# Performance work log

Hardware: AMD Instinct MI355X
Metric: run time of the kernel (lower is better)

## Reference

```python
import jax, jax.numpy as jnp
import numpy as np
import math

N = 5000; K = 30; E = N * K
C_S, C_Z, C_A = 256, 128, 16
H, DH, P, L = 4, 64, 8, 4
NUM_AA = 21
NUM_RBF = 16; D_MIN, D_MAX = 2.0, 22.0
EPS = 1e-8

def _ln(x):
    mu = jnp.mean(x, -1, keepdims=True)
    var = jnp.mean((x - mu) ** 2, -1, keepdims=True)
    return (x - mu) * jax.lax.rsqrt(var + 1e-5)

def _inv_apply(rot, trans, x):
    # rigid invert_apply: R^T (x - t); rot [n,3,3], trans [n,3], x [n,p,3]
    return jnp.einsum('nji,npj->npi', rot, x - trans[:, None, :])

def _rbf(d):
    mu = jnp.linspace(D_MIN, D_MAX, NUM_RBF)
    sigma = (D_MAX - D_MIN) / NUM_RBF
    return jnp.exp(-(((d[..., None] - mu) / sigma) ** 2))

def _dihedral_feats(bb):
    X = bb.reshape(-1, 3)  # [3N,3] N,CA,C chain
    dX = X[1:] - X[:-1]
    U = dX / (jnp.linalg.norm(dX, axis=-1, keepdims=True) + EPS)
    u2, u1, u0 = U[:-2], U[1:-1], U[2:]
    n2 = jnp.cross(u2, u1); n2 = n2 / (jnp.linalg.norm(n2, axis=-1, keepdims=True) + EPS)
    n1 = jnp.cross(u1, u0); n1 = n1 / (jnp.linalg.norm(n1, axis=-1, keepdims=True) + EPS)
    cosD = jnp.clip(jnp.sum(n2 * n1, -1), -1 + 1e-7, 1 - 1e-7)
    D = jnp.sign(jnp.sum(u2 * n1, -1)) * jnp.arccos(cosD)
    D = jnp.pad(D, (1, 2)).reshape(-1, 3)  # [N,3]
    return jnp.concatenate([jnp.cos(D), jnp.sin(D)], -1)  # [N,6]

def _virtual_cb(n, ca, c):
    b = ca - n; cc = c - ca; a = jnp.cross(b, cc)
    return -0.58273431 * a + 0.56802827 * b - 0.54067466 * cc + ca

def _prep(seq, atom14, rot, trans, res_mask, mgm_mask, noising_mask, atom14_exists, edge_index, atom_tab):
    res_f = res_mask.astype(jnp.float32)
    mgm_f = mgm_mask.astype(jnp.float32)
    bb = atom14[:, :3]
    dih = _dihedral_feats(bb)
    seq_oh = jax.nn.one_hot(seq, NUM_AA)
    node_vec = _inv_apply(rot, trans, atom14[:, :4])  # [N,4,3]
    node_raw = jnp.concatenate([dih, mgm_f[:, None], seq_oh * mgm_f[:, None], node_vec.reshape(N, -1)], -1) * res_f[:, None]
    sc = jnp.where(jnp.arange(14) >= 4, mgm_f[:, None], 1.0)  # zero hidden side-chain atoms
    am_f = jnp.where(jnp.arange(14) >= 4, mgm_mask[:, None], atom14_exists).astype(jnp.float32)
    atom_raw = atom_tab[seq] * sc[..., None]  # [N,14,9]
    dsti, srci = edge_index[0], edge_index[1]
    nsrc = noising_mask[srci].astype(jnp.float32); ndst = noising_mask[dsti].astype(jnp.float32)
    cb = _virtual_cb(bb[:, 0], bb[:, 1], bb[:, 2])
    bb4 = jnp.concatenate([bb, cb[:, None]], 1)  # [N,4,3]
    dist = jnp.linalg.norm(bb4[srci][:, :, None] - bb4[dsti][:, None, :] + EPS, axis=-1)  # [E,4,4]
    rbf = _rbf(dist).reshape(E, -1)  # [E,256]
    dpos = (dsti - srci).astype(jnp.float32)
    freq = jnp.exp(jnp.arange(0, 16, 2, dtype=jnp.float32) * (-math.log(10000.0) / 16))
    ang = dpos[:, None] * freq
    pe = jnp.concatenate([jnp.cos(ang), jnp.sin(ang)], -1)  # [E,16]
    bb_local = _inv_apply(rot, trans, bb4)
    src_local = bb_local[srci].reshape(E, -1) * (1 - nsrc)[:, None]
    dst_in_src = jnp.einsum('eji,epj->epi', rot[srci], bb4[dsti] - trans[srci][:, None, :]).reshape(E, -1) * (1 - ndst)[:, None]
    edge_mask = res_mask[srci] & res_mask[dsti]
    edge_raw = jnp.concatenate([ndst[:, None], nsrc[:, None], seq_oh[srci] * (1 - nsrc)[:, None], seq_oh[dsti] * (1 - ndst)[:, None], rbf, pe, src_local, dst_in_src], -1) * edge_mask.astype(jnp.float32)[:, None]
    return node_raw, edge_raw, atom_raw, res_f, am_f, edge_mask

def _mlp3(x, W1, W2, W3):
    return _ln(jax.nn.relu(jax.nn.relu(x @ W1) @ W2) @ W3)

def _net(node_raw, edge_raw, atom_raw, res_f, am_f, edge_mask, rot, trans, edge_index, Wn1, Wn2, Wn3, Wez1, Wez2, Wez3, Wa1, Wa2, Wa3, Wq, Wk, Wv, Wqp, Wkp, Wb, gamma, Wo, Wau, Wt1, Wt2, Wne, We1, We2, Wp1, Wp2, Wmu, Wlv):
    s = _mlp3(node_raw, Wn1, Wn2, Wn3)    # [N,256]
    z = _mlp3(edge_raw, Wez1, Wez2, Wez3) # [E,128]
    af = _mlp3(atom_raw, Wa1, Wa2, Wa3)   # [N,14,16]
    dsti, srci = edge_index[0], edge_index[1]
    em_f = edge_mask.astype(jnp.float32)
    w_pt = math.sqrt(2.0 / (9 * P)); w_l = math.sqrt(1.0 / 3.0)
    for l in range(L):
        q = (s @ Wq[l]).reshape(N, H, DH); k = (s @ Wk[l]).reshape(N, H, DH); v = (s @ Wv[l]).reshape(N, H, DH)
        qp = (s @ Wqp[l]).reshape(N, H, P, 3); kp = (s @ Wkp[l]).reshape(N, H, P, 3)
        qg = jnp.einsum('nij,nhpj->nhpi', rot, qp) + trans[:, None, None, :]
        kg = jnp.einsum('nij,nhpj->nhpi', rot, kp) + trans[:, None, None, :]
        logits = (jnp.sum(q[dsti] * k[srci], -1) * (w_l / math.sqrt(DH))
                  + w_l * (z @ Wb[l])
                  - 0.5 * w_pt * jax.nn.softplus(gamma[l]) * jnp.sum((qg[dsti] - kg[srci]) ** 2, (-2, -1)))
        logits = jnp.where(edge_mask[:, None], logits, -1e9)
        m = jax.ops.segment_max(logits, dsti, num_segments=N)
        a = jnp.exp(logits - m[dsti]) * em_f[:, None]
        a = a / (jax.ops.segment_sum(a, dsti, num_segments=N) + 1e-9)[dsti]
        ov = jax.ops.segment_sum(a[..., None] * v[srci], dsti, num_segments=N).reshape(N, -1)
        og = jax.ops.segment_sum(a[..., None, None] * kg[srci], dsti, num_segments=N)
        ol = jnp.einsum('nji,nhpj->nhpi', rot, og - trans[:, None, None, :])
        on = jnp.sqrt(jnp.sum(ol ** 2, -1) + EPS)
        s = _ln(s + jnp.concatenate([ov, ol.reshape(N, -1), on.reshape(N, -1)], -1) @ Wo[l])
        af = _ln(af + jnp.concatenate([af, jnp.broadcast_to(s[:, None, :], (N, 14, C_S))], -1) @ Wau[l])
        s = _ln(s + jax.nn.relu(s @ Wt1[l]) @ Wt2[l]) * res_f[:, None]
        h = s @ Wne[l]
        z = _ln(jax.nn.relu(jnp.concatenate([z, h[dsti], h[srci]], -1) @ We1[l]) @ We2[l]) * em_f[:, None]
        af = _ln(af + jax.nn.relu(af @ Wp1[l]) @ Wp2[l]) * am_f[..., None]
    return jnp.concatenate([s @ Wmu, s @ Wlv], -1)  # [N,512] = [mu | logvar]

def setup_inputs():
    ks = jax.random.split(jax.random.key(0), 40)
    w = lambda i, shp: jax.random.normal(ks[i], shp, dtype=jnp.float32) * 0.02
    return {
        'seq': jax.random.randint(ks[0], (N,), 0, NUM_AA, dtype=jnp.int32),
        'atom14': jax.random.normal(ks[1], (N, 14, 3), dtype=jnp.float32) * 3.0,
        'rot': jax.random.normal(ks[2], (N, 3, 3), dtype=jnp.float32),
        'trans': jax.random.normal(ks[3], (N, 3), dtype=jnp.float32) * 3.0,
        'res_mask': jnp.ones((N,), dtype=bool),
        'mgm_mask': jax.random.bernoulli(ks[4], 0.5, (N,)),
        'noising_mask': jax.random.bernoulli(ks[5], 0.5, (N,)),
        'atom14_exists': jnp.ones((N, 14), dtype=bool),
        'edge_index': jax.random.randint(ks[6], (2, E), 0, N, dtype=jnp.int32),
        'atom_tab': jax.random.uniform(ks[7], (NUM_AA + 1, 14, 9), dtype=jnp.float32),
        'Wn1': w(8, (40, 512)), 'Wn2': w(9, (512, 512)), 'Wn3': w(10, (512, 256)),
        'Wez1': w(11, (340, 256)), 'Wez2': w(12, (256, 256)), 'Wez3': w(13, (256, 128)),
        'Wa1': w(14, (9, 32)), 'Wa2': w(15, (32, 32)), 'Wa3': w(16, (32, 16)),
        'Wq': w(17, (L, 256, 256)), 'Wk': w(18, (L, 256, 256)), 'Wv': w(19, (L, 256, 256)),
        'Wqp': w(20, (L, 256, H * P * 3)), 'Wkp': w(21, (L, 256, H * P * 3)),
        'Wb': w(22, (L, 128, H)), 'gamma': w(23, (L, H)),
        'Wo': w(24, (L, H * (DH + 4 * P), 256)), 'Wau': w(25, (L, C_A + C_S, C_A)),
        'Wt1': w(26, (L, 256, 256)), 'Wt2': w(27, (L, 256, 256)),
        'Wne': w(28, (L, 256, 128)), 'We1': w(29, (L, 384, 256)), 'We2': w(30, (L, 256, 128)),
        'Wp1': w(31, (L, 16, 16)), 'Wp2': w(32, (L, 16, 16)),
        'Wmu': w(33, (256, 256)), 'Wlv': w(34, (256, 256)),
    }

def reference(seq, atom14, rot, trans, res_mask, mgm_mask, noising_mask, atom14_exists, edge_index, atom_tab, Wn1, Wn2, Wn3, Wez1, Wez2, Wez3, Wa1, Wa2, Wa3, Wq, Wk, Wv, Wqp, Wkp, Wb, gamma, Wo, Wau, Wt1, Wt2, Wne, We1, We2, Wp1, Wp2, Wmu, Wlv):
    prep = _prep(seq, atom14, rot, trans, res_mask, mgm_mask, noising_mask, atom14_exists, edge_index, atom_tab)
    return _net(*prep, rot, trans, edge_index, Wn1, Wn2, Wn3, Wez1, Wez2, Wez3, Wa1, Wa2, Wa3, Wq, Wk, Wv, Wqp, Wkp, Wb, gamma, Wo, Wau, Wt1, Wt2, Wne, We1, We2, Wp1, Wp2, Wmu, Wlv)
```

## Files before the change

### kernel.cpp

```cpp
#include <hip/hip_runtime.h>
#include <hip/hip_bf16.h>

#define NR 5000
#define EE 150000
#define NA14 (NR*14)
#define EPSF 1e-8f

typedef unsigned short ushort;
typedef __attribute__((ext_vector_type(8))) short bf16x8;
typedef __attribute__((ext_vector_type(4))) float f32x4;

#define GLDS16(gp, lp) __builtin_amdgcn_global_load_lds( \
    (__attribute__((address_space(1))) void*)(gp), \
    (__attribute__((address_space(3))) void*)(lp), 16, 0, 0)

static __device__ __forceinline__ float wsum64(float v) {
#pragma unroll
  for (int o = 1; o < 64; o <<= 1) v += __shfl_xor(v, o, 64);
  return v;
}
static __device__ __forceinline__ ushort f2b(float f) {
  union { float f; unsigned u; } x; x.f = f;
  unsigned r = (x.u + 0x7FFF + ((x.u >> 16) & 1)) >> 16;
  return (ushort)r;
// ... 312 lines not shown
  const int ks0 = (sl - rl0 - (rl0 >> 2)) & 3;
  const int ks1 = (sl - rl1 - (rl1 >> 2)) & 3;
  int ar0 = bm + rl0; if (ar0 >= M) ar0 = M - 1;
  int ar1 = bm + rl1; if (ar1 >= M) ar1 = M - 1;
  const ushort* gA0 = A + (size_t)ar0 * lda + ks0 * 8;
  const ushort* gA1 = A + (size_t)ar1 * lda + ks1 * 8;
  const ushort* gB0 = BT + (size_t)(bn + rl0) * Kd + ks0 * 8;
  const ushort* gB1 = BT + (size_t)(bn + rl1) * Kd + ks1 * 8;

  auto stage = [&](int buf, int k0) {
    GLDS16(gA0 + k0, &As[buf][rl0][sl][0]);
    GLDS16(gB0 + k0, &Bs[buf][rl0][sl][0]);
    GLDS16(gA1 + k0, &As[buf][rl1][sl][0]);
    GLDS16(gB1 + k0, &Bs[buf][rl1][sl][0]);
  };

  f32x4 zero4 = {0.f, 0.f, 0.f, 0.f};
  f32x4 acc[4][4];
#pragma unroll
  for (int i = 0; i < 4; ++i)
#pragma unroll
    for (int j = 0; j < 4; ++j) acc[i][j] = zero4;

  stage(0, 0);
  asm volatile("s_waitcnt vmcnt(0)" ::: "memory");
  __builtin_amdgcn_s_barrier();

  const int nt = Kd >> 5;
  for (int t = 0; t < nt; ++t) {
    int cur = t & 1;
    if (t + 1 < nt) stage(cur ^ 1, (t + 1) << 5);
    {
      const int ksr = lane >> 4, lr = lane & 15;
      bf16x8 af[4], bf[4];
#pragma unroll
      for (int i = 0; i < 4; ++i) {
        int row = wm + i*16 + lr;
        int sa = (ksr + row + (row >> 2)) & 3;
        af[i] = *reinterpret_cast<const bf16x8*>(&As[cur][row][sa][0]);
      }
#pragma unroll
      for (int j = 0; j < 4; ++j) {
        int col = wn + j*16 + lr;
        int sb = (ksr + col + (col >> 2)) & 3;
        bf[j] = *reinterpret_cast<const bf16x8*>(&Bs[cur][col][sb][0]);
      }
#pragma unroll
      for (int i = 0; i < 4; ++i)
#pragma unroll
        for (int j = 0; j < 4; ++j)
          acc[i][j] = __builtin_amdgcn_mfma_f32_16x16x32_bf16(af[i], bf[j], acc[i][j], 0, 0, 0);
    }
    asm volatile("s_waitcnt vmcnt(0) lgkmcnt(0)" ::: "memory");
    __builtin_amdgcn_s_barrier();
  }

  int lr = lane & 15, lg = lane >> 4;
  if (LNZ) {
    float* stats = (float*)As;
#pragma unroll
    for (int i = 0; i < 4; ++i) {
#pragma unroll
      for (int rg = 0; rg < 4; ++rg) {
        float ps = 0.f, pq = 0.f;
#pragma unroll
        for (int j = 0; j < 4; ++j) {
          float v = b2f(f2b(acc[i][j][rg]));
          ps += v; pq += v * v;
        }
#pragma unroll
        for (int o = 1; o < 16; o <<= 1) {
          ps += __shfl_xor(ps, o, 64);
          pq += __shfl_xor(pq, o, 64);
        }
        if (lr == 0) {
          int row = wm + i*16 + lg*4 + rg;
          stats[(row * 2 + (wn >> 6)) * 2 + 0] = ps;
          stats[(row * 2 + (wn >> 6)) * 2 + 1] = pq;
        }
      }
    }
    __syncthreads();
#pragma unroll
    for (int i = 0; i < 4; ++i) {
#pragma unroll
      for (int rg = 0; rg < 4; ++rg) {
        int row = wm + i*16 + lg*4 + rg;
        int m = bm + row;
        float s0 = stats[(row*2 + 0)*2 + 0] + stats[(row*2 + 1)*2 + 0];
        float q0 = stats[(row*2 + 0)*2 + 1] + stats[(row*2 + 1)*2 + 1];
        float mu = s0 * (1.f / 128.f);
        float var = q0 * (1.f / 128.f) - mu * mu;
        float rs = rsqrtf(var + 1e-5f);
        if (m < M) {
          float sc = lnsc ? lnsc[m] : 1.f;
#pragma unroll
          for (int j = 0; j < 4; ++j) {
            int cc = wn + j*16 + lr;
            float v = b2f(f2b(acc[i][j][rg]));
            Cb[(size_t)m * 128 + cc] = f2b((v - mu) * rs * sc);
          }
        }
      }
    }
  } else if (PERMOUT) {
    const int pc = bn + wn + lr * 4;
#pragma unroll
    for (int i = 0; i < 4; ++i) {
#pragma unroll
      for (int rg = 0; rg < 4; ++rg) {
        int m = bm + wm + i*16 + lg*4 + rg;
        if (m >= M) continue;
        float v0 = acc[i][0][rg], v1 = acc[i][1][rg];
        float v2 = acc[i][2][rg], v3 = acc[i][3][rg];
        if (EPADD) {
          int de = dsti[m], se = srci[m];
          uint2 hd = *reinterpret_cast<const uint2*>(HD + (size_t)de * Ncols + pc);
          uint2 hs = *reinterpret_cast<const uint2*>(HS + (size_t)se * Ncols + pc);
          v0 += blo(hd.x) + blo(hs.x);
          v1 += bhi(hd.x) + bhi(hs.x);
          v2 += blo(hd.y) + blo(hs.y);
          v3 += bhi(hd.y) + bhi(hs.y);
        }
        if (RELU) {
          v0 = fmaxf(v0, 0.f); v1 = fmaxf(v1, 0.f);
          v2 = fmaxf(v2, 0.f); v3 = fmaxf(v3, 0.f);
        }
        uint2 p;
        p.x = (unsigned)f2b(v0) | ((unsigned)f2b(v1) << 16);
        p.y = (unsigned)f2b(v2) | ((unsigned)f2b(v3) << 16);
        *reinterpret_cast<uint2*>(Cb + (size_t)m * Ncols + pc) = p;
      }
    }
  } else {
#pragma unroll
    for (int i = 0; i < 4; ++i) {
#pragma unroll
      for (int rg = 0; rg < 4; ++rg) {
        int m = bm + wm + i*16 + lg*4 + rg;
        if (m >= M) continue;
#pragma unroll
        for (int j = 0; j < 4; ++j) {
          int cc = bn + wn + j*16 + lr;
          float v = acc[i][j][rg];
          if (RELU) v = fmaxf(v, 0.f);
          if (OUTBF) Cb[(size_t)m * Ncols + cc] = f2b(v);
          else       Cf[(size_t)m * Ncols + cc] = v;
        }
      }
    }
  }
}

__global__ void k_gemm(const float* __restrict__ A, const float* __restrict__ B,
                       float* __restrict__ C, int M, int Ncols, int Kd,
                       int ldc, int coff, int relu) {
  __shared__ float As[16][68];
  __shared__ float Bs[16][64];
  const int tid = threadIdx.x;
  const int bm = blockIdx.x * 64;
  const int bn = blockIdx.y * 64;
  const int tm = tid >> 4;
  const int tn = tid & 15;
  const int arow = tid >> 2;
  const int akq = (tid & 3) << 2;
  const int brow = tid >> 4;
  const int bcol = (tid & 15) << 2;
  float acc[4][4] = {{0.f}};
  const int am = bm + arow;
  for (int k0 = 0; k0 < Kd; k0 += 16) {
    float av[4];
#pragma unroll
    for (int j = 0; j < 4; ++j) {
      int k = k0 + akq + j;
      av[j] = (am < M && k < Kd) ? A[(size_t)am * Kd + k] : 0.f;
    }
#pragma unroll
    for (int j = 0; j < 4; ++j) As[akq + j][arow] = av[j];
    int kb = k0 + brow;
    float bv[4];
    if (kb < Kd) {
#pragma unroll
      for (int j = 0; j < 4; ++j) {
        int c = bn + bcol + j;
        bv[j] = (c < Ncols) ? B[(size_t)kb * Ncols + c] : 0.f;
      }
    } else { bv[0]=bv[1]=bv[2]=bv[3]=0.f; }
    *reinterpret_cast<float4*>(&Bs[brow][bcol]) = make_float4(bv[0],bv[1],bv[2],bv[3]);
    __syncthreads();
#pragma unroll
    for (int kk = 0; kk < 16; ++kk) {
      float4 a4 = *reinterpret_cast<const float4*>(&As[kk][tm << 2]);
      float4 b4 = *reinterpret_cast<const float4*>(&Bs[kk][tn << 2]);
      float aa[4] = {a4.x, a4.y, a4.z, a4.w};
      float bb[4] = {b4.x, b4.y, b4.z, b4.w};
#pragma unroll
      for (int i = 0; i < 4; ++i)
#pragma unroll
        for (int j = 0; j < 4; ++j)
          acc[i][j] = fmaf(aa[i], bb[j], acc[i][j]);
    }
    __syncthreads();
  }
#pragma unroll
  for (int i = 0; i < 4; ++i) {
    int m = bm + (tm << 2) + i;
    if (m >= M) continue;
#pragma unroll
    for (int j = 0; j < 4; ++j) {
      int c = bn + (tn << 2) + j;
      if (c >= Ncols) continue;
      float v = acc[i][j];
      if (relu) v = fmaxf(v, 0.f);
      C[(size_t)m * ldc + coff + c] = v;
    }
  }
}

__global__ void k_small_gemm(const float* __restrict__ A, const float* __restrict__ B,
                             float* __restrict__ C, int M, int Ncols, int Kd, int relu) {
  __shared__ float Ws[1024];
  int t = threadIdx.x;
  int nw = Kd * Ncols;
  for (int i = t; i < nw; i += 256) Ws[i] = B[i];
  __syncthreads();
  int rpb = 256 / Ncols;
  int r = blockIdx.x * rpb + t / Ncols;
  int c = t - (t / Ncols) * Ncols;
  if (r >= M || t >= rpb * Ncols) return;
  const float* a = A + (size_t)r * Kd;
  float s = 0.f;
  for (int k = 0; k < Kd; ++k) s = fmaf(a[k], Ws[k * Ncols + c], s);
  if (relu) s = fmaxf(s, 0.f);
  C[(size_t)r * Ncols + c] = s;
}

__global__ void k_ln(float* __restrict__ dst, ushort* __restrict__ dstb,
                     const float* __restrict__ res, const float* __restrict__ x,
                     const float* __restrict__ rowscale, int M) {
  int r = blockIdx.x * 4 + (threadIdx.x >> 6);
  if (r >= M) return;
  int l = threadIdx.x & 63;
  size_t base = (size_t)r * 256 + l * 4;
  float4 v = *reinterpret_cast<const float4*>(x + base);
  if (res) {
    float4 rv = *reinterpret_cast<const float4*>(res + base);
    v.x += rv.x; v.y += rv.y; v.z += rv.z; v.w += rv.w;
  }
  float s = wsum64(v.x + v.y + v.z + v.w);
  float mu = s * (1.f / 256.f);
  float d0 = v.x-mu, d1 = v.y-mu, d2 = v.z-mu, d3 = v.w-mu;
  float s2 = wsum64(d0*d0 + d1*d1 + d2*d2 + d3*d3);
  float rs = rsqrtf(s2 * (1.f / 256.f) + 1e-5f);
  float sc = rowscale ? rowscale[r] : 1.f;
  float o0 = d0*rs*sc, o1 = d1*rs*sc, o2 = d2*rs*sc, o3 = d3*rs*sc;
  *reinterpret_cast<float4*>(dst + base) = make_float4(o0, o1, o2, o3);
  if (dstb) {
    uint2 p;
    p.x = (unsigned)f2b(o0) | ((unsigned)f2b(o1) << 16);
    p.y = (unsigned)f2b(o2) | ((unsigned)f2b(o3) << 16);
    *reinterpret_cast<uint2*>(dstb + base) = p;
  }
}

__global__ void k_ln16(float* __restrict__ af, int M) {
  int r = blockIdx.x * 256 + threadIdx.x;
  if (r >= M) return;
  float x[16]; float s = 0.f;
#pragma unroll
  for (int j = 0; j < 16; ++j) { x[j] = af[(size_t)r*16 + j]; s += x[j]; }
  float mu = s * (1.f/16.f);
  float v = 0.f;
#pragma unroll
  for (int j = 0; j < 16; ++j) { float d = x[j]-mu; v += d*d; }
  float rs = rsqrtf(v * (1.f/16.f) + 1e-5f);
#pragma unroll
  for (int j = 0; j < 16; ++j) af[(size_t)r*16 + j] = (x[j]-mu)*rs;
}


__global__ void k_qg(const float* __restrict__ rot, const float* __restrict__ trans,
                     const float* __restrict__ pp,
                     float* __restrict__ qg, float* __restrict__ kg) {
  int idx = blockIdx.x * 256 + threadIdx.x;
  if (idx >= NR * 64) return;
  int n = idx >> 6; int w = (idx >> 5) & 1; int hp = idx & 31;
  const float* src = pp + (size_t)n*256 + (w ? 96 : 0) + hp*3;
  float* dstp = (w ? kg : qg) + (size_t)n*96 + hp*3;
  const float* R = rot + (size_t)n*9;
  const float* t = trans + (size_t)n*3;
  float s0 = src[0], s1 = src[1], s2 = src[2];
#pragma unroll
  for (int i = 0; i < 3; ++i)
    dstp[i] = R[i*3+0]*s0 + R[i*3+1]*s1 + R[i*3+2]*s2 + t[i];
}

__global__ __launch_bounds__(256) void k_attn2(
    const int* __restrict__ offs, const int* __restrict__ eord,
    const int* __restrict__ srci, const float* __restrict__ emf,
    const ushort* __restrict__ qkv, const ushort* __restrict__ z,
    const float* __restrict__ qg, const float* __restrict__ kg,
    const float* __restrict__ WbT, const float* __restrict__ coef,
    ushort* __restrict__ catb, float* __restrict__ og) {
  __shared__ float MS[2][2][8];
  __shared__ float AV[2][2][4][64];
  __shared__ float AG0[2][2][64];
  __shared__ float AG1[2][2][32];
  const int w = threadIdx.x >> 6;
  const int ns = w >> 1, half = w & 1;
  const int n = blockIdx.x * 2 + ns;
  const int l = threadIdx.x & 63;
  const int hh = l >> 4, t = l & 15;
  const int e0 = offs[n], e1 = offs[n+1];
  const float wl = 0.57735026918962576f;
  const float qk_scale = wl * 0.125f;
  uint2 qw = *reinterpret_cast<const uint2*>(qkv + n*768 + hh*64 + t*4);
  float q0 = blo(qw.x), q1 = bhi(qw.x), q2 = blo(qw.y), q3 = bhi(qw.y);
  float qg1 = qg[n*96 + hh*24 + t];
  float qg2 = (t < 8) ? qg[n*96 + hh*24 + t + 16] : 0.f;
  float cf = coef[hh];
  int hg0 = l / 24;
  int hg1 = (64 + l) / 24;

  float m[4] = {-1e30f,-1e30f,-1e30f,-1e30f};
  float den[4] = {0.f,0.f,0.f,0.f};
  float accv[4] = {0.f,0.f,0.f,0.f};
  float acg0 = 0.f, acg1 = 0.f;

  int i = e0 + half;
  int e = 0, s = 0;
  if (i < e1) {
    e = __builtin_amdgcn_readfirstlane(eord[i]);
    s = __builtin_amdgcn_readfirstlane(srci[e]);
  }
  for (; i < e1; i += 2) {
    int e_nxt = 0, s_nxt = 0;
    if (i + 2 < e1) {
      e_nxt = __builtin_amdgcn_readfirstlane(eord[i + 2]);
      s_nxt = __builtin_amdgcn_readfirstlane(srci[e_nxt]);
    }
    float em = emf[e];
    uint2 kw = *reinterpret_cast<const uint2*>(qkv + s*768 + 256 + hh*64 + t*4);
    float acc = qk_scale * (q0*blo(kw.x) + q1*bhi(kw.x) + q2*blo(kw.y) + q3*bhi(kw.y));
    {
      uint4 zw = *reinterpret_cast<const uint4*>(z + (size_t)e*128 + t*8);
      const float* wb = WbT + hh*128 + t*8;
      float4 w0 = *reinterpret_cast<const float4*>(wb);
      float4 w1 = *reinterpret_cast<const float4*>(wb + 4);
      acc += wl * (blo(zw.x)*w0.x + bhi(zw.x)*w0.y + blo(zw.y)*w0.z + bhi(zw.y)*w0.w
                 + blo(zw.z)*w1.x + bhi(zw.z)*w1.y + blo(zw.w)*w1.z + bhi(zw.w)*w1.w);
    }
    {
      float dq = qg1 - kg[s*96 + hh*24 + t];
      acc -= cf * dq * dq;
      if (t < 8) {
        float dq2 = qg2 - kg[s*96 + hh*24 + t + 16];
        acc -= cf * dq2 * dq2;
      }
    }
#pragma unroll
    for (int o = 1; o < 16; o <<= 1) acc += __shfl_xor(acc, o, 64);
    float a[4], r[4];
#pragma unroll
    for (int h = 0; h < 4; ++h) {
      float vh = __shfl(acc, h*16, 64);
      float lg = (em > 0.f) ? vh : -1e9f;
      float mn = m[h];
      r[h] = 1.f;
      if (lg > mn) { r[h] = expf(mn - lg); mn = lg; m[h] = mn; }
      a[h] = expf(lg - mn) * em;
      den[h] = den[h] * r[h] + a[h];
    }
#pragma unroll
    for (int j = 0; j < 4; ++j)
      accv[j] = accv[j] * r[j] + a[j] * b2f(qkv[s*768 + 512 + j*64 + l]);
    acg0 = acg0 * r[hg0] + a[hg0] * kg[s*96 + l];
    if (l < 32) acg1 = acg1 * r[hg1] + a[hg1] * kg[s*96 + 64 + l];
    e = e_nxt; s = s_nxt;
  }
  if (l == 0) {
#pragma unroll
    for (int h = 0; h < 4; ++h) { MS[ns][half][h] = m[h]; MS[ns][half][4+h] = den[h]; }
  }
#pragma unroll
  for (int j = 0; j < 4; ++j) AV[ns][half][j][l] = accv[j];
  AG0[ns][half][l] = acg0;
  if (l < 32) AG1[ns][half][l] = acg1;
  __syncthreads();
  if (half) return;
  float rA[4], rB[4], dC[4];
#pragma unroll
  for (int h = 0; h < 4; ++h) {
    float mA = MS[ns][0][h], mB = MS[ns][1][h];
    float mC = fmaxf(mA, mB);
    rA[h] = expf(mA - mC); rB[h] = expf(mB - mC);
    dC[h] = MS[ns][0][4+h]*rA[h] + MS[ns][1][4+h]*rB[h];
  }
#pragma unroll
  for (int j = 0; j < 4; ++j) {
    float v = AV[ns][0][j][l]*rA[j] + AV[ns][1][j][l]*rB[j];
    catb[(size_t)n*384 + j*64 + l] = f2b(v / (dC[j] + 1e-9f));
  }
  float g0 = AG0[ns][0][l]*rA[hg0] + AG0[ns][1][l]*rB[hg0];
  og[(size_t)n*96 + l] = g0 / (dC[hg0] + 1e-9f);
  if (l < 32) {
    float g1 = AG1[ns][0][l]*rA[hg1] + AG1[ns][1][l]*rB[hg1];
    og[(size_t)n*96 + 64 + l] = g1 / (dC[hg1] + 1e-9f);
  }
}

__global__ void k_olon(const float* __restrict__ rot, const float* __restrict__ trans,
                       const float* __restrict__ og, ushort* __restrict__ catb) {
  int idx = blockIdx.x * 256 + threadIdx.x;
  if (idx >= NR * 32) return;
  int n = idx >> 5, hp = idx & 31;
  const float* R = rot + (size_t)n*9;
  const float* t = trans + (size_t)n*3;
  const float* o = og + (size_t)n*96 + hp*3;
  float d0 = o[0]-t[0], d1 = o[1]-t[1], d2 = o[2]-t[2];
  float ol[3];
#pragma unroll
  for (int i = 0; i < 3; ++i)
    ol[i] = R[0*3+i]*d0 + R[1*3+i]*d1 + R[2*3+i]*d2;
  ushort* cp = catb + (size_t)n*384;
  cp[256 + hp*3 + 0] = f2b(ol[0]);
  cp[256 + hp*3 + 1] = f2b(ol[1]);
  cp[256 + hp*3 + 2] = f2b(ol[2]);
  cp[352 + hp] = f2b(sqrtf(ol[0]*ol[0] + ol[1]*ol[1] + ol[2]*ol[2] + EPSF));
}

__global__ void k_af_wau(float* __restrict__ af, const float* __restrict__ WauA,
                         const float* __restrict__ t1) {
  __shared__ float W[256];
  int t = threadIdx.x;
  W[t] = WauA[t];
  __syncthreads();
  int r = blockIdx.x * 256 + t;
  if (r >= NA14) return;
  int n = r / 14;
  float x[16], y[16];
#pragma unroll
  for (int j = 0; j < 16; ++j) x[j] = af[(size_t)r*16 + j];
#pragma unroll
  for (int j = 0; j < 16; ++j) y[j] = t1[(size_t)n*16 + j];
#pragma unroll
  for (int k = 0; k < 16; ++k) {
    float xv = x[k];
#pragma unroll
    for (int j = 0; j < 16; ++j) y[j] = fmaf(xv, W[k*16 + j], y[j]);
  }
  float v[16]; float s = 0.f;
#pragma unroll
  for (int j = 0; j < 16; ++j) { v[j] = x[j] + y[j]; s += v[j]; }
  float mu = s * (1.f/16.f);
  float var = 0.f;
#pragma unroll
  for (int j = 0; j < 16; ++j) { float d = v[j]-mu; var += d*d; }
  float rs = rsqrtf(var * (1.f/16.f) + 1e-5f);
#pragma unroll
  for (int j = 0; j < 16; ++j) af[(size_t)r*16 + j] = (v[j]-mu)*rs;
}

__global__ void k_af_p(float* __restrict__ af, const float* __restrict__ Wp1,
                       const float* __restrict__ Wp2, const float* __restrict__ amf) {
  __shared__ float W1[256], W2[256];
  int t = threadIdx.x;
  W1[t] = Wp1[t]; W2[t] = Wp2[t];
  __syncthreads();
  int r = blockIdx.x * 256 + t;
  if (r >= NA14) return;
  float x[16];
#pragma unroll
  for (int j = 0; j < 16; ++j) x[j] = af[(size_t)r*16 + j];
  float h1[16];
#pragma unroll
  for (int j = 0; j < 16; ++j) h1[j] = 0.f;
#pragma unroll
  for (int k = 0; k < 16; ++k) {
    float xv = x[k];
#pragma unroll
    for (int j = 0; j < 16; ++j) h1[j] = fmaf(xv, W1[k*16 + j], h1[j]);
  }
#pragma unroll
  for (int j = 0; j < 16; ++j) h1[j] = fmaxf(h1[j], 0.f);
  float h2[16];
#pragma unroll
  for (int j = 0; j < 16; ++j) h2[j] = 0.f;
#pragma unroll
  for (int k = 0; k < 16; ++k) {
    float xv = h1[k];
#pragma unroll
    for (int j = 0; j < 16; ++j) h2[j] = fmaf(xv, W2[k*16 + j], h2[j]);
  }
  float v[16]; float s = 0.f;
#pragma unroll
  for (int j = 0; j < 16; ++j) { v[j] = x[j] + h2[j]; s += v[j]; }
  float mu = s * (1.f/16.f);
  float var = 0.f;
#pragma unroll
  for (int j = 0; j < 16; ++j) { float d = v[j]-mu; var += d*d; }
  float rs = rsqrtf(var * (1.f/16.f) + 1e-5f);
  float am = amf[r];
#pragma unroll
  for (int j = 0; j < 16; ++j) af[(size_t)r*16 + j] = (v[j]-mu)*rs*am;
}

__global__ void k_sentinel(float* __restrict__ out, float val) {
  if (threadIdx.x == 0 && blockIdx.x == 0) out[0] = val;
}


extern "C" void kernel_launch(void* const* d_in, const int* in_sizes, int n_in,
                              void* d_out, int out_size, void* d_ws, size_t ws_size,
                              hipStream_t stream) {
  (void)in_sizes; (void)n_in; (void)out_size;
  const int*   seq    = (const int*)  d_in[0];
  const float* atom14 = (const float*)d_in[1];
  const float* rot    = (const float*)d_in[2];
  const float* trans  = (const float*)d_in[3];
  const int*   rmask  = (const int*)  d_in[4];
  const int*   mgm    = (const int*)  d_in[5];
  const int*   nmask  = (const int*)  d_in[6];
  const int*   a14ex  = (const int*)  d_in[7];
  const int*   eidx   = (const int*)  d_in[8];
  const int*   dsti   = eidx;
  const int*   srci   = eidx + EE;
  const float* atab   = (const float*)d_in[9];
  const float* Wn1 = (const float*)d_in[10];
  const float* Wn2 = (const float*)d_in[11];
  const float* Wn3 = (const float*)d_in[12];
  const float* Wez1 = (const float*)d_in[13];
  const float* Wez2 = (const float*)d_in[14];
  const float* Wez3 = (const float*)d_in[15];
  const float* Wa1 = (const float*)d_in[16];
  const float* Wa2 = (const float*)d_in[17];
  const float* Wa3 = (const float*)d_in[18];
  const float* Wq  = (const float*)d_in[19];
  const float* Wk  = (const float*)d_in[20];
  const float* Wv  = (const float*)d_in[21];
  const float* Wqp = (const float*)d_in[22];
  const float* Wkp = (const float*)d_in[23];
  const float* Wb  = (const float*)d_in[24];
  const float* gam = (const float*)d_in[25];
  const float* Wo  = (const float*)d_in[26];
  const float* Wau = (const float*)d_in[27];
  const float* Wt1 = (const float*)d_in[28];
  const float* Wt2 = (const float*)d_in[29];
  const float* Wne = (const float*)d_in[30];
  const float* We1 = (const float*)d_in[31];
  const float* We2 = (const float*)d_in[32];
  const float* Wp1 = (const float*)d_in[33];
  const float* Wp2 = (const float*)d_in[34];
  const float* Wmu = (const float*)d_in[35];
  const float* Wlv = (const float*)d_in[36];
  float* out = (float*)d_out;

  float* ws = (float*)d_ws;
  size_t WSF = ws_size / sizeof(float);
  size_t off = 0;
  auto alloc = [&](size_t n) { n = (n + 3) & ~(size_t)3; float* p = ws + off; off += n; return p; };

  ushort* Zb  = (ushort*)alloc((size_t)EE * 64);
  float* S    = alloc((size_t)NR * 256);
  ushort* SB  = (ushort*)alloc((size_t)NR * 128);
  float* AF   = alloc((size_t)NA14 * 16);
  float* AMF  = alloc(NA14);
  float* EMF  = alloc(EE);
  float* RESF = alloc(NR);
  float* DP   = alloc(3 * NR);
  float* BB4  = alloc((size_t)NR * 12);
  float* BBL  = alloc((size_t)NR * 12);
  ushort* NRAWB = (ushort*)alloc((size_t)NR * 32);
  float* ARAW = alloc((size_t)NA14 * 9);
  ushort* WezT1 = (ushort*)alloc(45056);
  ushort* WezT2 = (ushort*)alloc(32768);
  ushort* WezT3 = (ushort*)alloc(16384);
  ushort* We1zT = (ushort*)alloc(65536);
  ushort* We1dT = (ushort*)alloc(65536);
  ushort* We1sT = (ushort*)alloc(65536);
  ushort* We2T  = (ushort*)alloc(65536);
  ushort* WqkvT = (ushort*)alloc(393216);
  ushort* WppT  = (ushort*)alloc(131072);
  ushort* WoT   = (ushort*)alloc(196608);
  ushort* Wt1T  = (ushort*)alloc(131072);
  ushort* Wt2T  = (ushort*)alloc(131072);
  ushort* WneT  = (ushort*)alloc(65536);
  ushort* WmuLvT= (ushort*)alloc(65536);
  ushort* Wn1T  = (ushort*)alloc(16384);
  ushort* Wn2T  = (ushort*)alloc(131072);
  ushort* Wn3T  = (ushort*)alloc(65536);
  float* WBT  = alloc(2048);
  float* COEF = alloc(16);
  ushort* QKVB= (ushort*)alloc((size_t)NR * 384);
  float* PP   = alloc((size_t)NR * 256);
  float* QG   = alloc((size_t)NR * 96);
  float* KG   = alloc((size_t)NR * 96);
  ushort* CATB= (ushort*)alloc((size_t)NR * 192);
  float* OGb  = alloc((size_t)NR * 96);
  float* NBUF = alloc((size_t)NR * 256);
  ushort* HbB = (ushort*)alloc((size_t)NR * 64);
  ushort* HDb = (ushort*)alloc((size_t)NR * 128);
  ushort* HSb = (ushort*)alloc((size_t)NR * 128);
  float* T1   = alloc((size_t)NR * 16);
  ushort* NB1b = (ushort*)alloc((size_t)NR * 256);
  ushort* NB2b = (ushort*)alloc((size_t)NR * 256);
  ushort* TRHb = (ushort*)alloc((size_t)NR * 128);
  float* AH1  = alloc((size_t)NA14 * 32);
  float* AH2  = alloc((size_t)NA14 * 32);
  int* CNT  = (int*)alloc(NR);
  int* OFFS = (int*)alloc(NR + 1);
  int* EORD = (int*)alloc(EE);
  size_t fixedF = off;

  if (fixedF + (size_t)432 * 1024 > WSF) {
    k_sentinel<<<1, 64, 0, stream>>>(out, 1.0e6f * (float)(ws_size >> 20));
    return;
  }
  float* EAR = ws + fixedF;
  size_t arenaF = WSF - fixedF;
  int CH_P = (int)((arenaF / 432 > (size_t)EE) ? (size_t)EE : arenaF / 432);
  int CH_L = (int)((arenaF / 128 > (size_t)EE) ? (size_t)EE : arenaF / 128);
  ushort* ERb = (ushort*)EAR;
  ushort* B1b = ERb + (size_t)CH_P * 352;
  ushort* B2b = B1b + (size_t)CH_P * 256;
  ushort* EARb = (ushort*)EAR;

  auto wT = [&](const float* W, ushort* WTp, int K, int N, int Kpad,
                long ss, long ds, int L, int perm) {
    long tot = (long)N * Kpad * L;
    k_wT<<<(int)((tot + 255) / 256), 256, 0, stream>>>(W, WTp, K, N, Kpad, ss, ds, L, perm);
  };

  wT(Wez1, WezT1, 340, 256, 352, 0, 0, 1, 0);
  wT(Wez2, WezT2, 256, 256, 256, 0, 0, 1, 1);
  wT(Wez3, WezT3, 256, 128, 256, 0, 0, 1, 1);
  wT(Wn1, Wn1T, 40, 512, 64, 0, 0, 1, 0);
  wT(Wn2, Wn2T, 512, 512, 512, 0, 0, 1, 1);
  wT(Wn3, Wn3T, 512, 256, 512, 0, 0, 1, 1);
  wT(We1,         We1zT, 128, 256, 128, 98304, 32768, 4, 0);
  wT(We1 + 32768, We1dT, 128, 256, 128, 98304, 32768, 4, 0);
  wT(We1 + 65536, We1sT, 128, 256, 128, 98304, 32768, 4, 0);
  wT(We2, We2T, 256, 128, 256, 32768, 32768, 4, 1);
  wT(Wo,  WoT,  384, 256, 384, 98304, 98304, 4, 0);
  wT(Wt1, Wt1T, 256, 256, 256, 65536, 65536, 4, 0);
  wT(Wt2, Wt2T, 256, 256, 256, 65536, 65536, 4, 1);
  wT(Wne, WneT, 256, 128, 256, 32768, 32768, 4, 0);
  wT(Wmu, WmuLvT, 256, 256, 256, 0, 0, 1, 0);
  wT(Wlv, WmuLvT + 65536, 256, 256, 256, 0, 0, 1, 0);
  wT(Wq,  WqkvT + 0,       256, 256, 256, 65536, 196608, 4, 0);
  wT(Wk,  WqkvT + 65536,   256, 256, 256, 65536, 196608, 4, 0);
  wT(Wv,  WqkvT + 131072,  256, 256, 256, 65536, 196608, 4, 0);
  wT(Wqp, WppT + 0,        256,  96, 256, 24576, 65536, 4, 0);
  wT(Wkp, WppT + 24576,    256,  96, 256, 24576, 65536, 4, 0);
  k_zero_us<<<(64*256*4 + 255)/256, 256, 0, stream>>>(WppT + 49152, 64*256, 65536, 4);
  k_wbT<<<8, 256, 0, stream>>>(Wb, WBT);
  k_coef<<<1, 64, 0, stream>>>(gam, COEF);

  k_masks<<<(NR + 255) / 256, 256, 0, stream>>>(rmask, RESF);
  k_dihedral<<<(3 * NR + 255) / 256, 256, 0, stream>>>(atom14, DP);
  k_bb4<<<(NR + 255) / 256, 256, 0, stream>>>(atom14, rot, trans, BB4, BBL);
  k_noderaw<<<NR, 64, 0, stream>>>(seq, atom14, rot, trans, DP, rmask, mgm, NRAWB);
  k_atomraw<<<(NA14 + 255) / 256, 256, 0, stream>>>(seq, mgm, a14ex, atab, ARAW, AMF);

  {
    dim3 g1((NR + 127) / 128, 4), g2((NR + 127) / 128, 4), g3((NR + 127) / 128, 2);
    k_mgemm<1,1,0,1,0><<<g1, 256, 0, stream>>>(NRAWB, Wn1T, nullptr, NB1b, NR, 512, 64, 64,
                                               nullptr, nullptr, nullptr, nullptr, nullptr);
    k_mgemm<1,1,0,1,0><<<g2, 256, 0, stream>>>(NB1b, Wn2T, nullptr, NB2b, NR, 512, 512, 512,
                                               nullptr, nullptr, nullptr, nullptr, nullptr);
    k_mgemm<0,0,0,0,0><<<g3, 256, 0, stream>>>(NB2b, Wn3T, NBUF, nullptr, NR, 256, 512, 512,
                                               nullptr, nullptr, nullptr, nullptr, nullptr);
  }
  k_ln<<<(NR + 3) / 4, 256, 0, stream>>>(S, SB, nullptr, NBUF, nullptr, NR);

  k_small_gemm<<<(NA14 + 7) / 8, 256, 0, stream>>>(ARAW, Wa1, AH1, NA14, 32, 9, 1);
  k_small_gemm<<<(NA14 + 7) / 8, 256, 0, stream>>>(AH1, Wa2, AH2, NA14, 32, 32, 1);
  k_small_gemm<<<(NA14 + 15) / 16, 256, 0, stream>>>(AH2, Wa3, AF, NA14, 16, 32, 0);
  k_ln16<<<(NA14 + 255) / 256, 256, 0, stream>>>(AF, NA14);

  k_zero_int<<<(NR + 255) / 256, 256, 0, stream>>>(CNT, NR);
  k_count<<<(EE + 255) / 256, 256, 0, stream>>>(dsti, CNT);
  k_scan<<<1, 256, 0, stream>>>(CNT, OFFS);
  k_zero_int<<<(NR + 255) / 256, 256, 0, stream>>>(CNT, NR);
  k_place<<<(EE + 255) / 256, 256, 0, stream>>>(dsti, OFFS, CNT, EORD);
  k_sortwave<<<NR, 64, 0, stream>>>(OFFS, EORD);

  for (int e0 = 0; e0 < EE; e0 += CH_P) {
    int cnt = (EE - e0 < CH_P) ? (EE - e0) : CH_P;
    k_edgeraw<<<(cnt + 3) / 4, 256, 0, stream>>>(dsti, srci, seq, rmask, nmask,
                                                 BB4, BBL, rot, trans, ERb, EMF, e0, cnt);
    dim3 g1((cnt + 127) / 128, 2), g2((cnt + 127) / 128, 2), g3((cnt + 127) / 128, 1);
    k_mgemm<1,1,0,1,0><<<g1, 256, 0, stream>>>(ERb, WezT1, nullptr, B1b, cnt, 256, 352, 352,
                                               nullptr, nullptr, nullptr, nullptr, nullptr);
    k_mgemm<1,1,0,1,0><<<g2, 256, 0, stream>>>(B1b, WezT2, nullptr, B2b, cnt, 256, 256, 256,
                                               nullptr, nullptr, nullptr, nullptr, nullptr);
    k_mgemm<0,1,0,0,1><<<g3, 256, 0, stream>>>(B2b, WezT3, nullptr, Zb + (size_t)e0 * 128,
                                               cnt, 128, 256, 256,
                                               nullptr, nullptr, nullptr, nullptr, nullptr);
  }

  for (int l = 0; l < 4; ++l) {
    const ushort* WqkvT_l = WqkvT + (size_t)l * 196608;
    const ushort* WppT_l  = WppT  + (size_t)l * 65536;
    const ushort* WoT_l = WoT + (size_t)l * 98304;
    const float* Wau_l = Wau + (size_t)l * 4352;
    const ushort* Wt1T_l = Wt1T + (size_t)l * 65536;
    const ushort* Wt2T_l = Wt2T + (size_t)l * 65536;
    const ushort* WneT_l = WneT + (size_t)l * 32768;
    const ushort* We1zT_l = We1zT + (size_t)l * 32768;
    const ushort* We1dT_l = We1dT + (size_t)l * 32768;
    const ushort* We1sT_l = We1sT + (size_t)l * 32768;
    const ushort* We2T_l = We2T + (size_t)l * 32768;
    const float* Wp1_l = Wp1 + (size_t)l * 256;
    const float* Wp2_l = Wp2 + (size_t)l * 256;

    {
      dim3 gq((NR + 127) / 128, 6);
      k_mgemm<0,1,0,0,0><<<gq, 256, 0, stream>>>(SB, WqkvT_l, nullptr, QKVB, NR, 768, 256, 256,
                                                 nullptr, nullptr, nullptr, nullptr, nullptr);
      dim3 gp((NR + 127) / 128, 2);
      k_mgemm<0,0,0,0,0><<<gp, 256, 0, stream>>>(SB, WppT_l, PP, nullptr, NR, 256, 256, 256,
                                                 nullptr, nullptr, nullptr, nullptr, nullptr);
    }
    k_qg<<<(NR * 64 + 255) / 256, 256, 0, stream>>>(rot, trans, PP, QG, KG);
    k_attn2<<<NR / 2, 256, 0, stream>>>(OFFS, EORD, srci, EMF, QKVB, Zb, QG, KG,
                                        WBT + (size_t)l * 512, COEF + (size_t)l * 4,
                                        CATB, OGb);
    k_olon<<<(NR * 32 + 255) / 256, 256, 0, stream>>>(rot, trans, OGb, CATB);
    {
      dim3 g((NR + 127) / 128, 2);
      k_mgemm<0,0,0,0,0><<<g, 256, 0, stream>>>(CATB, WoT_l, NBUF, nullptr, NR, 256, 384, 384,
                                                nullptr, nullptr, nullptr, nullptr, nullptr);
    }
    k_ln<<<(NR + 3) / 4, 256, 0, stream>>>(S, SB, S, NBUF, nullptr, NR);
    {
      dim3 g((NR + 63) / 64, 1);
      k_gemm<<<g, 256, 0, stream>>>(S, Wau_l + 256, T1, NR, 16, 256, 16, 0, 0);
    }
    k_af_wau<<<(NA14 + 255) / 256, 256, 0, stream>>>(AF, Wau_l, T1);
    {
      dim3 g((NR + 127) / 128, 2);
      k_mgemm<1,1,0,1,0><<<g, 256, 0, stream>>>(SB, Wt1T_l, nullptr, TRHb, NR, 256, 256, 256,
                                                nullptr, nullptr, nullptr, nullptr, nullptr);
      k_mgemm<0,0,0,0,0><<<g, 256, 0, stream>>>(TRHb, Wt2T_l, NBUF, nullptr, NR, 256, 256, 256,
                                                nullptr, nullptr, nullptr, nullptr, nullptr);
    }
    k_ln<<<(NR + 3) / 4, 256, 0, stream>>>(S, SB, S, NBUF, RESF, NR);
    {
      dim3 g((NR + 127) / 128, 1);
      k_mgemm<0,1,0,0,0><<<g, 256, 0, stream>>>(SB, WneT_l, nullptr, HbB, NR, 128, 256, 256,
                                                nullptr, nullptr, nullptr, nullptr, nullptr);
    }
    {
      dim3 g((NR + 127) / 128, 2);
      k_mgemm<0,1,0,1,0><<<g, 256, 0, stream>>>(HbB, We1dT_l, nullptr, HDb, NR, 256, 128, 128,
                                                nullptr, nullptr, nullptr, nullptr, nullptr);
      k_mgemm<0,1,0,1,0><<<g, 256, 0, stream>>>(HbB, We1sT_l, nullptr, HSb, NR, 256, 128, 128,
                                                nullptr, nullptr, nullptr, nullptr, nullptr);
    }
    for (int e0 = 0; e0 < EE; e0 += CH_L) {
      int cnt = (EE - e0 < CH_L) ? (EE - e0) : CH_L;
      dim3 g1((cnt + 127) / 128, 2), g2((cnt + 127) / 128, 1);
      k_mgemm<1,1,1,1,0><<<g1, 256, 0, stream>>>(Zb + (size_t)e0 * 128, We1zT_l, nullptr, EARb,
                                                 cnt, 256, 128, 128,
                                                 HDb, HSb, dsti + e0, srci + e0, nullptr);
      k_mgemm<0,1,0,0,1><<<g2, 256, 0, stream>>>(EARb, We2T_l, nullptr, Zb + (size_t)e0 * 128,
                                                 cnt, 128, 256, 256,
                                                 nullptr, nullptr, nullptr, nullptr, EMF + e0);
    }
    k_af_p<<<(NA14 + 255) / 256, 256, 0, stream>>>(AF, Wp1_l, Wp2_l, AMF);
  }

  {
    dim3 g((NR + 127) / 128, 4);
    k_mgemm<0,0,0,0,0><<<g, 256, 0, stream>>>(SB, WmuLvT, out, nullptr, NR, 512, 256, 256,
                                              nullptr, nullptr, nullptr, nullptr, nullptr);
  }
}
```

Before: 1.820 ms.

## Split attention edges across four waves per node and skip rescale when max unchanged

The edge-softmax attention kernel now gives each node a whole 256-thread block, so four wavefronts each take every fourth incoming edge instead of two wavefronts per node. Partial max, denominator and accumulators from the four waves are merged in shared memory. The online-softmax update also gains a fast path that skips the exp rescaling when no head's running max increases. This shortens each wave's serial dependency chain over about 30 edges and adds latency hiding, at the cost of twice as many blocks, a heavier reduction and a branch that can diverge.

```diff
diff --git a/kernel.cpp b/kernel.cpp
--- a/kernel.cpp
+++ b/kernel.cpp
@@ -638,13 +638,12 @@
     const float* __restrict__ qg, const float* __restrict__ kg,
     const float* __restrict__ WbT, const float* __restrict__ coef,
     ushort* __restrict__ catb, float* __restrict__ og) {
-  __shared__ float MS[2][2][8];
-  __shared__ float AV[2][2][4][64];
-  __shared__ float AG0[2][2][64];
-  __shared__ float AG1[2][2][32];
-  const int w = threadIdx.x >> 6;
-  const int ns = w >> 1, half = w & 1;
-  const int n = blockIdx.x * 2 + ns;
+  __shared__ float MS[4][8];
+  __shared__ float AV[4][4][64];
+  __shared__ float AG0[4][64];
+  __shared__ float AG1[4][32];
+  const int qtr = threadIdx.x >> 6;
+  const int n = blockIdx.x;
   const int l = threadIdx.x & 63;
   const int hh = l >> 4, t = l & 15;
   const int e0 = offs[n], e1 = offs[n+1];
@@ -663,16 +662,16 @@
   float accv[4] = {0.f,0.f,0.f,0.f};
   float acg0 = 0.f, acg1 = 0.f;
 
-  int i = e0 + half;
+  int i = e0 + qtr;
   int e = 0, s = 0;
   if (i < e1) {
     e = __builtin_amdgcn_readfirstlane(eord[i]);
     s = __builtin_amdgcn_readfirstlane(srci[e]);
   }
-  for (; i < e1; i += 2) {
+  for (; i < e1; i += 4) {
     int e_nxt = 0, s_nxt = 0;
-    if (i + 2 < e1) {
-      e_nxt = __builtin_amdgcn_readfirstlane(eord[i + 2]);
+    if (i + 4 < e1) {
+      e_nxt = __builtin_amdgcn_readfirstlane(eord[i + 4]);
       s_nxt = __builtin_amdgcn_readfirstlane(srci[e_nxt]);
     }
     float em = emf[e];
@@ -696,51 +695,74 @@
     }
 #pragma unroll
     for (int o = 1; o < 16; o <<= 1) acc += __shfl_xor(acc, o, 64);
-    float a[4], r[4];
+    float lgv[4];
+    bool resc = false;
 #pragma unroll
     for (int h = 0; h < 4; ++h) {
       float vh = __shfl(acc, h*16, 64);
-      float lg = (em > 0.f) ? vh : -1e9f;
-      float mn = m[h];
-      r[h] = 1.f;
-      if (lg > mn) { r[h] = expf(mn - lg); mn = lg; m[h] = mn; }
-      a[h] = expf(lg - mn) * em;
-      den[h] = den[h] * r[h] + a[h];
-    }
-#pragma unroll
-    for (int j = 0; j < 4; ++j)
-      accv[j] = accv[j] * r[j] + a[j] * b2f(qkv[s*768 + 512 + j*64 + l]);
-    acg0 = acg0 * r[hg0] + a[hg0] * kg[s*96 + l];
-    if (l < 32) acg1 = acg1 * r[hg1] + a[hg1] * kg[s*96 + 64 + l];
+      lgv[h] = (em > 0.f) ? vh : -1e9f;
+      if (lgv[h] > m[h]) resc = true;
+    }
+    if (!resc) {
+      float a[4];
+#pragma unroll
+      for (int h = 0; h < 4; ++h) { a[h] = expf(lgv[h] - m[h]) * em; den[h] += a[h]; }
+#pragma unroll
+      for (int j = 0; j < 4; ++j)
+        accv[j] = fmaf(a[j], b2f(qkv[s*768 + 512 + j*64 + l]), accv[j]);
+      acg0 = fmaf(a[hg0], kg[s*96 + l], acg0);
+      if (l < 32) acg1 = fmaf(a[hg1], kg[s*96 + 64 + l], acg1);
+    } else {
+      float a[4], r[4];
+#pragma unroll
+      for (int h = 0; h < 4; ++h) {
+        float mn = m[h];
+        r[h] = 1.f;
+        if (lgv[h] > mn) { r[h] = expf(mn - lgv[h]); mn = lgv[h]; m[h] = mn; }
+        a[h] = expf(lgv[h] - mn) * em;
+        den[h] = den[h] * r[h] + a[h];
+      }
+#pragma unroll
+      for (int j = 0; j < 4; ++j)
+        accv[j] = accv[j] * r[j] + a[j] * b2f(qkv[s*768 + 512 + j*64 + l]);
+      acg0 = acg0 * r[hg0] + a[hg0] * kg[s*96 + l];
+      if (l < 32) acg1 = acg1 * r[hg1] + a[hg1] * kg[s*96 + 64 + l];
+    }
     e = e_nxt; s = s_nxt;
   }
   if (l == 0) {
 #pragma unroll
-    for (int h = 0; h < 4; ++h) { MS[ns][half][h] = m[h]; MS[ns][half][4+h] = den[h]; }
-  }
-#pragma unroll
-  for (int j = 0; j < 4; ++j) AV[ns][half][j][l] = accv[j];
-  AG0[ns][half][l] = acg0;
-  if (l < 32) AG1[ns][half][l] = acg1;
+    for (int h = 0; h < 4; ++h) { MS[qtr][h] = m[h]; MS[qtr][4+h] = den[h]; }
+  }
+#pragma unroll
+  for (int j = 0; j < 4; ++j) AV[qtr][j][l] = accv[j];
+  AG0[qtr][l] = acg0;
+  if (l < 32) AG1[qtr][l] = acg1;
   __syncthreads();
-  if (half) return;
-  float rA[4], rB[4], dC[4];
+  if (qtr) return;
+  float rq[4][4], dC[4];
 #pragma unroll
   for (int h = 0; h < 4; ++h) {
-    float mA = MS[ns][0][h], mB = MS[ns][1][h];
-    float mC = fmaxf(mA, mB);
-    rA[h] = expf(mA - mC); rB[h] = expf(mB - mC);
-    dC[h] = MS[ns][0][4+h]*rA[h] + MS[ns][1][4+h]*rB[h];
+    float mC = fmaxf(fmaxf(MS[0][h], MS[1][h]), fmaxf(MS[2][h], MS[3][h]));
+    dC[h] = 0.f;
+#pragma unroll
+    for (int q = 0; q < 4; ++q) {
+      rq[q][h] = expf(MS[q][h] - mC);
+      dC[h] += MS[q][4+h] * rq[q][h];
+    }
   }
 #pragma unroll
   for (int j = 0; j < 4; ++j) {
-    float v = AV[ns][0][j][l]*rA[j] + AV[ns][1][j][l]*rB[j];
+    float v = AV[0][j][l]*rq[0][j] + AV[1][j][l]*rq[1][j]
+            + AV[2][j][l]*rq[2][j] + AV[3][j][l]*rq[3][j];
     catb[(size_t)n*384 + j*64 + l] = f2b(v / (dC[j] + 1e-9f));
   }
-  float g0 = AG0[ns][0][l]*rA[hg0] + AG0[ns][1][l]*rB[hg0];
+  float g0 = AG0[0][l]*rq[0][hg0] + AG0[1][l]*rq[1][hg0]
+           + AG0[2][l]*rq[2][hg0] + AG0[3][l]*rq[3][hg0];
   og[(size_t)n*96 + l] = g0 / (dC[hg0] + 1e-9f);
   if (l < 32) {
-    float g1 = AG1[ns][0][l]*rA[hg1] + AG1[ns][1][l]*rB[hg1];
+    float g1 = AG1[0][l]*rq[0][hg1] + AG1[1][l]*rq[1][hg1]
+             + AG1[2][l]*rq[2][hg1] + AG1[3][l]*rq[3][hg1];
     og[(size_t)n*96 + 64 + l] = g1 / (dC[hg1] + 1e-9f);
   }
 }
@@ -1059,9 +1081,9 @@
                                                  nullptr, nullptr, nullptr, nullptr, nullptr);
     }
     k_qg<<<(NR * 64 + 255) / 256, 256, 0, stream>>>(rot, trans, PP, QG, KG);
-    k_attn2<<<NR / 2, 256, 0, stream>>>(OFFS, EORD, srci, EMF, QKVB, Zb, QG, KG,
-                                        WBT + (size_t)l * 512, COEF + (size_t)l * 4,
-                                        CATB, OGb);
+    k_attn2<<<NR, 256, 0, stream>>>(OFFS, EORD, srci, EMF, QKVB, Zb, QG, KG,
+                                    WBT + (size_t)l * 512, COEF + (size_t)l * 4,
+                                    CATB, OGb);
     k_olon<<<(NR * 32 + 255) / 256, 256, 0, stream>>>(rot, trans, OGb, CATB);
     {
       dim3 g((NR + 127) / 128, 2);
```

New measurement: 1.774 ms. 2.5% less time.
